# Kernel tuning notes

Hardware: AMD Instinct MI355X
Metric: run time of the kernel (lower is better)

## Reference

```python
import jax, jax.numpy as jnp
import numpy as np

B, T, D, H, O = 64, 2048, 1024, 1024, 1024


def setup_inputs() -> dict:
    key = jax.random.key(0)
    ks = jax.random.split(key, 7)
    std = 1.0 / np.sqrt(H)
    u = lambda k, shape: jax.random.uniform(k, shape, jnp.float32, -std, std)
    return {
        "x": jax.random.normal(ks[0], (B, T, D), jnp.float32),
        "Wx": u(ks[1], (3 * H, D)),
        "bx": u(ks[2], (3 * H,)),
        "Wh": u(ks[3], (3 * H, H)),
        "bh": u(ks[4], (3 * H,)),
        "Wf": u(ks[5], (O, H)),
        "bf": u(ks[6], (O,)),
    }


def _gru_forward(x, Wx, bx, Wh, bh, Wf, bf):
    # Precompute input projections for all timesteps: [B, T, 3H]
    x_proj = jnp.einsum('btd,gd->btg', x, Wx) + bx

    def step(h, xp_t):
        # xp_t: [B, 3H], h: [B, H]
        h_proj = h @ Wh.T + bh
        x_r, x_u, x_n = jnp.split(xp_t, 3, axis=1)
        h_r, h_u, h_n = jnp.split(h_proj, 3, axis=1)
        reset = jax.nn.sigmoid(x_r + h_r)
        update = jax.nn.sigmoid(x_u + h_u)
        new = jnp.tanh(x_n + reset * h_n)
        hy = update * h + (1.0 - update) * new
        return hy, None

    h0 = jnp.zeros((x.shape[0], Wh.shape[1]), x.dtype)
    h_last, _ = jax.lax.scan(step, h0, jnp.swapaxes(x_proj, 0, 1))
    logits = h_last @ Wf.T + bf
    return jax.nn.log_softmax(logits, axis=-1)


def reference(x, Wx, bx, Wh, bh, Wf, bf):
    return _gru_forward(x, Wx, bx, Wh, bh, Wf, bf)
```

## Files before the change

### kernel.cpp

```cpp
#include <hip/hip_runtime.h>
#include <hip/hip_bf16.h>


#define Bb 64
#define Tt 2048
#define Dd 1024
#define Hh 1024

typedef __attribute__((ext_vector_type(8))) short bf16x8;
typedef __attribute__((ext_vector_type(4))) float f32x4;

__device__ __forceinline__ short f2bf(float x) {
    __hip_bfloat16 h = __float2bfloat16(x);
    return __builtin_bit_cast(short, h);
}
__device__ __forceinline__ float bf2f(unsigned short u) {
    return __builtin_bit_cast(float, (unsigned)u << 16);
}
__device__ __forceinline__ bf16x8 pack8(float4 a, float4 b) {
    bf16x8 f;
    f[0] = f2bf(a.x); f[1] = f2bf(a.y); f[2] = f2bf(a.z); f[3] = f2bf(a.w);
    f[4] = f2bf(b.x); f[5] = f2bf(b.y); f[6] = f2bf(b.z); f[7] = f2bf(b.w);
    return f;
}
__device__ __forceinline__ unsigned long long ald64(const void* p) {
    return __hip_atomic_load((const unsigned long long*)p, __ATOMIC_RELAXED,
                             __HIP_MEMORY_SCOPE_AGENT);
}
__device__ __forceinline__ unsigned aldu32(const unsigned* p) {
    return __hip_atomic_load(p, __ATOMIC_RELAXED, __HIP_MEMORY_SCOPE_AGENT);
}

__global__ void wcvt(const float* __restrict__ a, unsigned short* __restrict__ o, long n) {
    long i = ((long)blockIdx.x * blockDim.x + threadIdx.x) * 8;
    long stride = (long)gridDim.x * blockDim.x * 8;
    for (; i < n; i += stride)
        *(bf16x8*)(o + i) = pack8(*(const float4*)(a + i), *(const float4*)(a + i + 4));
}

__global__ __launch_bounds__(256)
void xp_gemm(const float* __restrict__ x, const unsigned short* __restrict__ Wxb,
             unsigned short* __restrict__ xp, int t0) {
    __shared__ unsigned short As[64][40];
    const int tid = threadIdx.x;
    const int wave = tid >> 6, l = tid & 63, lm = l & 15, lk = l >> 4;
    const int slot = blockIdx.y;
    const int t = t0 + slot;
    const int n0w = blockIdx.x * 128 + wave * 32;

    f32x4 acc[4][2] = {};
#pragma unroll 1
    for (int k0 = 0; k0 < 1024; k0 += 32) {
        __syncthreads();
        {
            const int r = tid >> 2, kq = (tid & 3) * 8;
            const float* p = x + (size_t)r * Tt * Dd + (size_t)t * Dd + k0 + kq;
            *(bf16x8*)&As[r][kq] = pack8(*(const float4*)p, *(const float4*)(p + 4));
        }
        __syncthreads();
        bf16x8 bfr[2];
#pragma unroll
        for (int nt = 0; nt < 2; ++nt)
            bfr[nt] = *(const bf16x8*)(Wxb + (size_t)(n0w + nt * 16 + lm) * 1024 + k0 + lk * 8);
#pragma unroll
        for (int mt = 0; mt < 4; ++mt) {
            const bf16x8 af = *(const bf16x8*)&As[mt * 16 + lm][lk * 8];
            acc[mt][0] = __builtin_amdgcn_mfma_f32_16x16x32_bf16(af, bfr[0], acc[mt][0], 0, 0, 0);
            acc[mt][1] = __builtin_amdgcn_mfma_f32_16x16x32_bf16(af, bfr[1], acc[mt][1], 0, 0, 0);
        }
    }
#pragma unroll
    for (int mt = 0; mt < 4; ++mt)
#pragma unroll
        for (int nt = 0; nt < 2; ++nt)
#pragma unroll
            for (int i = 0; i < 4; ++i) {
                const int b = mt * 16 + lk * 4 + i;
                const int n = n0w + nt * 16 + lm;
                xp[((size_t)slot * 64 + b) * 3072 + n] = (unsigned short)f2bf(acc[mt][nt][i]);
            }
}

__global__ __launch_bounds__(512, 2)
void gru_scan6(const float* __restrict__ Wh, const float* __restrict__ bx,
               const float* __restrict__ bh, unsigned short* __restrict__ hl2,
               unsigned short* __restrict__ hmall,
               float* __restrict__ hstate, float* __restrict__ hfinal,
               const unsigned short* __restrict__ xp, int t0, int tend) {
    const int tid = threadIdx.x;
    const int w = tid >> 6, l = tid & 63, lm = l & 15, lk = l >> 4;
    const int bid = blockIdx.x;
    const int g = bid & 7, c = bid >> 3;
    const int bg0 = g * 8, j0 = c * 32;
    const int kb = w * 128;

    __shared__ float comb[8][32][100];
    __shared__ float bxv[96], bhv[96];

    if (tid < 96) {
        const int g3 = tid >> 5, jj = tid & 31;
        bxv[tid] = bx[g3 * 1024 + j0 + jj];
        bhv[tid] = bh[g3 * 1024 + j0 + jj];
    }
    const int grow = tid >> 4, jp = (tid & 15) * 2;
    float hp0 = 0.f, hp1 = 0.f;
    if (tid < 128) {
        const float2 h2 = *(const float2*)(hstate + (size_t)(bg0 + grow) * 1024 + j0 + jp);
        hp0 = h2.x; hp1 = h2.y;
    }

    bf16x8 wf[6][4];
#pragma unroll
    for (int nt = 0; nt < 6; ++nt) {
        const int n96 = nt * 16 + lm, g3 = n96 >> 5, jj = n96 & 31;
        const float* rp = Wh + (size_t)(g3 * 1024 + j0 + jj) * 1024 + kb + lk * 8;
#pragma unroll
        for (int ks = 0; ks < 4; ++ks)
            wf[nt][ks] = pack8(*(const float4*)(rp + ks * 32), *(const float4*)(rp + ks * 32 + 4));
    }
    __syncthreads();

    unsigned xa0 = 0, xa1 = 0, xa2 = 0, xb0 = 0, xb1 = 0, xb2 = 0;
    if (tid < 128) {
        const unsigned short* xr = xp + ((size_t)0 * 64 + bg0 + grow) * 3072 + j0 + jp;
        xa0 = *(const unsigned*)(xr);
        xa1 = *(const unsigned*)(xr + 1024);
        xa2 = *(const unsigned*)(xr + 2048);
    }

    const int row_a = (lm < 8) ? lm : 7;
    unsigned long long rr0, rr1, rr2, rr3, rr4, rr5, rr6, rr7;
    int useMall = 0;

#define L2LOAD(P)                                                              \
    asm volatile(                                                              \
        "global_load_dwordx2 %[a0], %[ad], off sc0\n\t"                        \
        "global_load_dwordx2 %[a1], %[ad], off offset:8 sc0\n\t"               \
        "global_load_dwordx2 %[a2], %[ad], off offset:64 sc0\n\t"              \
        "global_load_dwordx2 %[a3], %[ad], off offset:72 sc0\n\t"              \
        "global_load_dwordx2 %[a4], %[ad], off offset:128 sc0\n\t"             \
        "global_load_dwordx2 %[a5], %[ad], off offset:136 sc0\n\t"             \
        "global_load_dwordx2 %[a6], %[ad], off offset:192 sc0\n\t"             \
        "global_load_dwordx2 %[a7], %[ad], off offset:200 sc0\n\t"             \
        "s_waitcnt vmcnt(0)"                                                   \
        : [a0] "=&v"(rr0), [a1] "=&v"(rr1), [a2] "=&v"(rr2), [a3] "=&v"(rr3),  \
          [a4] "=&v"(rr4), [a5] "=&v"(rr5), [a6] "=&v"(rr6), [a7] "=&v"(rr7)   \
        : [ad] "v"(P)                                                          \
        : "memory")

#pragma unroll 1
    for (int t = t0; t < tend; ++t) {
        const size_t hoff = (size_t)(t & 1) * 65536 + (size_t)g * 8192
                            + (size_t)row_a * 1024 + kb + lk * 8;
        const unsigned long long TAGM = 0x0000000100000001ull;
        const unsigned long long tagrep =
            (unsigned long long)((unsigned)(t >> 1) & 1u) * TAGM;

        if (!useMall) {
            const unsigned short* pl = hl2 + hoff;
            int spins = 0;
            for (;;) {
                L2LOAD(pl);
                const unsigned long long bad =
                    ((rr0 ^ tagrep) | (rr1 ^ tagrep) | (rr2 ^ tagrep) | (rr3 ^ tagrep) |
                     (rr4 ^ tagrep) | (rr5 ^ tagrep) | (rr6 ^ tagrep) | (rr7 ^ tagrep)) & TAGM;
                if (__builtin_expect(__all(bad == 0), 1)) break;
                if (++spins > 256) { useMall = 1; break; }
            }
        }
        if (useMall) {
            const unsigned short* pm = hmall + hoff;
            for (;;) {
                rr0 = ald64(pm);       rr1 = ald64(pm + 4);
                rr2 = ald64(pm + 32);  rr3 = ald64(pm + 36);
                rr4 = ald64(pm + 64);  rr5 = ald64(pm + 68);
                rr6 = ald64(pm + 96);  rr7 = ald64(pm + 100);
                const unsigned long long bad =
                    ((rr0 ^ tagrep) | (rr1 ^ tagrep) | (rr2 ^ tagrep) | (rr3 ^ tagrep) |
                     (rr4 ^ tagrep) | (rr5 ^ tagrep) | (rr6 ^ tagrep) | (rr7 ^ tagrep)) & TAGM;
                if (__builtin_expect(__all(bad == 0), 1)) break;
            }
        }

        if (tid < 128 && t + 1 < tend) {
            const unsigned short* xr = xp + ((size_t)(t + 1 - t0) * 64 + bg0 + grow) * 3072 + j0 + jp;
            xb0 = *(const unsigned*)(xr);
            xb1 = *(const unsigned*)(xr + 1024);
            xb2 = *(const unsigned*)(xr + 2048);
        }

        f32x4 acc[6] = {};
#define KSTEP(KA, KB, KS)                                                       \
        do {                                                                    \
            struct U { unsigned long long a, b; } u{KA, KB};                    \
            const bf16x8 af = __builtin_bit_cast(bf16x8, u);                    \
            _Pragma("unroll")                                                   \
            for (int nt = 0; nt < 6; ++nt)                                      \
                acc[nt] = __builtin_amdgcn_mfma_f32_16x16x32_bf16(              \
                    af, wf[nt][KS], acc[nt], 0, 0, 0);                          \
        } while (0)
        KSTEP(rr0, rr1, 0); KSTEP(rr2, rr3, 1); KSTEP(rr4, rr5, 2); KSTEP(rr6, rr7, 3);
#undef KSTEP

        if (lk < 2) {
#pragma unroll
            for (int nt = 0; nt < 6; ++nt)
#pragma unroll
                for (int i = 0; i < 4; ++i)
                    comb[w][lk * 4 + i][nt * 16 + lm] = acc[nt][i];
        }
        asm volatile("s_waitcnt lgkmcnt(0)\ns_barrier" ::: "memory");

        if (tid < 128) {
            float s00 = 0, s10 = 0, s20 = 0, s01 = 0, s11 = 0, s21 = 0;
#pragma unroll
            for (int ww = 0; ww < 8; ++ww) {
                s00 += comb[ww][grow][jp];      s01 += comb[ww][grow][jp + 1];
                s10 += comb[ww][grow][32 + jp]; s11 += comb[ww][grow][32 + jp + 1];
                s20 += comb[ww][grow][64 + jp]; s21 += comb[ww][grow][64 + jp + 1];
            }
            const float xr0 = bf2f((unsigned short)xa0) + bxv[jp];
            const float xr1 = bf2f((unsigned short)(xa0 >> 16)) + bxv[jp + 1];
            const float xu0 = bf2f((unsigned short)xa1) + bxv[32 + jp];
            const float xu1 = bf2f((unsigned short)(xa1 >> 16)) + bxv[32 + jp + 1];
            const float xn0 = bf2f((unsigned short)xa2) + bxv[64 + jp];
            const float xn1 = bf2f((unsigned short)(xa2 >> 16)) + bxv[64 + jp + 1];
            const float r0 = 1.0f / (1.0f + __expf(-(xr0 + s00 + bhv[jp])));
            const float r1 = 1.0f / (1.0f + __expf(-(xr1 + s01 + bhv[jp + 1])));
            const float u0 = 1.0f / (1.0f + __expf(-(xu0 + s10 + bhv[32 + jp])));
            const float u1 = 1.0f / (1.0f + __expf(-(xu1 + s11 + bhv[32 + jp + 1])));
            const float z0 = xn0 + r0 * (s20 + bhv[64 + jp]);
            const float z1 = xn1 + r1 * (s21 + bhv[64 + jp + 1]);
            const float e0 = __expf(2.0f * z0), e1 = __expf(2.0f * z1);
            const float n0 = 1.0f - 2.0f / (e0 + 1.0f);
            const float n1 = 1.0f - 2.0f / (e1 + 1.0f);
            const float hy0 = u0 * hp0 + (1.0f - u0) * n0;
            const float hy1 = u1 * hp1 + (1.0f - u1) * n1;
            hp0 = hy0; hp1 = hy1;
            const unsigned tagn = ((unsigned)(t + 1) >> 1) & 1u;
            const unsigned v0 = ((unsigned)(unsigned short)f2bf(hy0) & 0xFFFEu) | tagn;
            const unsigned pk = ((unsigned)(unsigned short)f2bf(hy1) << 16) | v0;
            const size_t soff = (size_t)((t + 1) & 1) * 65536 + (size_t)g * 8192
                                + (size_t)grow * 1024 + j0 + jp;
            *(volatile unsigned*)(hl2 + soff) = pk;
            __hip_atomic_store((unsigned*)(hmall + soff), pk, __ATOMIC_RELAXED,
                               __HIP_MEMORY_SCOPE_AGENT);
            if (t == tend - 1)
                *(float2*)(hstate + (size_t)(bg0 + grow) * 1024 + j0 + jp) = make_float2(hy0, hy1);
            if (t == Tt - 1)
                *(float2*)(hfinal + (size_t)(bg0 + grow) * 1024 + j0 + jp) = make_float2(hy0, hy1);
            xa0 = xb0; xa1 = xb1; xa2 = xb2;
        }
        asm volatile("s_barrier" ::: "memory");
    }
#undef L2LOAD
}

template <bool RING>
__global__ __launch_bounds__(256, 1)
void gru_scan(const float* __restrict__ x,
              const float* __restrict__ Wx, const float* __restrict__ bx,
              const float* __restrict__ Wh, const float* __restrict__ bh,
              unsigned short* __restrict__ hbuf, float* __restrict__ hfinal,
              unsigned short* __restrict__ ring, unsigned* __restrict__ flags) {
    const int tid = threadIdx.x;
    const int w   = tid >> 6;
    const int l   = tid & 63;
    const int bid = blockIdx.x;
    const int g   = bid & 1;
    const int c   = bid >> 1;
    const int bg0 = g * 32;
    const int j0  = c * 8;

    __shared__ float comb[4][32][24];
    __shared__ float hp[32][8];
    __shared__ float bxv[24], bhv[24];

    hp[tid >> 3][tid & 7] = 0.0f;
    if (tid < 24) {
        const int gate = tid >> 3, jj = tid & 7;
        bxv[tid] = bx[gate * 1024 + j0 + jj];
        bhv[tid] = bh[gate * 1024 + j0 + jj];
    }

    const int lm = l & 15;
    const int lk = l >> 4;
    const int wb = w * 512;
    bf16x8 bfr[2][16];
    {
        const float* Wbase = (w < 2) ? Wx : Wh;
        const int krel = (w < 2) ? wb : (wb - 1024);
#pragma unroll
        for (int nt = 0; nt < 2; ++nt) {
            int row24 = nt * 16 + lm;
            if (row24 > 23) row24 = 23;
            const int gate = row24 >> 3, jj = row24 & 7;
            const float* rp = Wbase + (size_t)(gate * 1024 + j0 + jj) * 1024 + krel + lk * 8;
#pragma unroll
            for (int ks = 0; ks < 16; ++ks) {
                float4 a = *(const float4*)(rp + ks * 32);
                float4 b = *(const float4*)(rp + ks * 32 + 4);
                bfr[nt][ks] = pack8(a, b);
            }
        }
    }
    __syncthreads();

    if (RING) {
        if (tid < 128) {
            const int e = c * 256 + tid * 2;
            const int rl = e >> 10, col = e & 1023;
#pragma unroll
            for (int s = 0; s < 4; ++s) {
                const float2 xv = *(const float2*)(x + ((size_t)(bg0 + rl) * Tt + s) * Dd + col);
                unsigned pk = (unsigned)(unsigned short)f2bf(xv.x)
                            | ((unsigned)(unsigned short)f2bf(xv.y) << 16);
                __hip_atomic_store((unsigned*)(ring + (size_t)s * 65536
                                               + (size_t)(bg0 + rl) * 1024 + col),
                                   pk, __ATOMIC_RELAXED, __HIP_MEMORY_SCOPE_AGENT);
            }
        }
        asm volatile("s_waitcnt vmcnt(0)" ::: "memory");
        __syncthreads();
        if (tid == 0)
            __hip_atomic_store(&flags[g * 128 + c], 1u, __ATOMIC_RELAXED,
                               __HIP_MEMORY_SCOPE_AGENT);
        if (tid < 128) {
            const unsigned* f = flags + g * 128 + tid;
            while (aldu32(f) < 1u) __builtin_amdgcn_s_sleep(1);
        }
        asm volatile("" ::: "memory");
        __syncthreads();
    }

#pragma unroll 1
    for (int t = 0; t < Tt; ++t) {
        const unsigned short* hcur = hbuf + (size_t)(t & 1) * Bb * Hh;

        if (RING && tid < 128) {
            const int sp = t + 4;
            if (sp < Tt) {
                const int e = c * 256 + tid * 2;
                const int rl = e >> 10, col = e & 1023;
                const float2 xv = *(const float2*)(x + ((size_t)(bg0 + rl) * Tt + sp) * Dd + col);
                unsigned pk = (unsigned)(unsigned short)f2bf(xv.x)
                            | ((unsigned)(unsigned short)f2bf(xv.y) << 16);
                __hip_atomic_store((unsigned*)(ring + (size_t)(sp & 7) * 65536
                                               + (size_t)(bg0 + rl) * 1024 + col),
                                   pk, __ATOMIC_RELAXED, __HIP_MEMORY_SCOPE_AGENT);
            }
        }

        if (w >= 2 && t > 0) {
            const unsigned tgt = (unsigned)(t + 1);
            const unsigned* f0 = flags + g * 128 + l;
            const unsigned* f1 = f0 + 64;
            while (aldu32(f0) < tgt || aldu32(f1) < tgt) __builtin_amdgcn_s_sleep(1);
        }
        asm volatile("" ::: "memory");

        f32x4 acc[2][2] = {};
        if (RING || w >= 2) {
            const unsigned short* src;
            int colb;
            if (w < 2) { src = ring + (size_t)(t & 7) * 65536; colb = wb; }
            else       { src = hcur;                           colb = wb - 1024; }
#pragma unroll
            for (int half = 0; half < 2; ++half) {
                unsigned long long stg[8][2][2];
#pragma unroll
                for (int k8 = 0; k8 < 8; ++k8) {
                    const int ks = half * 8 + k8;
#pragma unroll
                    for (int mt = 0; mt < 2; ++mt) {
                        const unsigned short* p = src + (size_t)(bg0 + mt * 16 + lm) * 1024
                                                  + colb + ks * 32 + lk * 8;
                        stg[k8][mt][0] = ald64(p);
                        stg[k8][mt][1] = ald64(p + 4);
                    }
                }
#pragma unroll
                for (int k8 = 0; k8 < 8; ++k8) {
                    const int ks = half * 8 + k8;
#pragma unroll
                    for (int mt = 0; mt < 2; ++mt) {
                        struct { unsigned long long a, b; } u{stg[k8][mt][0], stg[k8][mt][1]};
                        bf16x8 af = __builtin_bit_cast(bf16x8, u);
                        acc[mt][0] = __builtin_amdgcn_mfma_f32_16x16x32_bf16(af, bfr[0][ks], acc[mt][0], 0, 0, 0);
                        acc[mt][1] = __builtin_amdgcn_mfma_f32_16x16x32_bf16(af, bfr[1][ks], acc[mt][1], 0, 0, 0);
                    }
                }
            }
        } else {
#pragma unroll
            for (int ks = 0; ks < 16; ++ks) {
#pragma unroll
                for (int mt = 0; mt < 2; ++mt) {
                    const size_t row = (size_t)(bg0 + mt * 16 + lm);
                    const size_t off = (row * Tt + t) * Dd + wb + ks * 32 + lk * 8;
                    float4 a = *(const float4*)(x + off);
                    float4 b = *(const float4*)(x + off + 4);
                    bf16x8 af = pack8(a, b);
                    acc[mt][0] = __builtin_amdgcn_mfma_f32_16x16x32_bf16(af, bfr[0][ks], acc[mt][0], 0, 0, 0);
                    acc[mt][1] = __builtin_amdgcn_mfma_f32_16x16x32_bf16(af, bfr[1][ks], acc[mt][1], 0, 0, 0);
                }
            }
        }

#pragma unroll
        for (int mt = 0; mt < 2; ++mt)
#pragma unroll
            for (int nt = 0; nt < 2; ++nt) {
                const int n = nt * 16 + lm;
                if (n < 24) {
#pragma unroll
                    for (int i = 0; i < 4; ++i)
                        comb[w][mt * 16 + lk * 4 + i][n] = acc[mt][nt][i];
                }
            }
        __syncthreads();

        {
            const int b = tid >> 3, j = tid & 7;
            const float rz = comb[0][b][j] + comb[1][b][j] + comb[2][b][j] + comb[3][b][j]
                             + bxv[j] + bhv[j];
            const float uz = comb[0][b][8 + j] + comb[1][b][8 + j] + comb[2][b][8 + j]
                             + comb[3][b][8 + j] + bxv[8 + j] + bhv[8 + j];
            const float nx = comb[0][b][16 + j] + comb[1][b][16 + j] + bxv[16 + j];
            const float nh = comb[2][b][16 + j] + comb[3][b][16 + j] + bhv[16 + j];
            const float r  = 1.0f / (1.0f + __expf(-rz));
            const float u  = 1.0f / (1.0f + __expf(-uz));
            const float zz = nx + r * nh;
            const float e2 = __expf(2.0f * zz);
            const float nv = 1.0f - 2.0f / (e2 + 1.0f);
            const float hold = hp[b][j];
            const float hy = u * hold + (1.0f - u) * nv;
            hp[b][j] = hy;
            unsigned short* hn = hbuf + (size_t)((t + 1) & 1) * Bb * Hh
                                 + (size_t)(bg0 + b) * 1024 + j0 + j;
            __hip_atomic_store(hn, (unsigned short)f2bf(hy), __ATOMIC_RELAXED,
                               __HIP_MEMORY_SCOPE_AGENT);
            if (t == Tt - 1) hfinal[(size_t)(bg0 + b) * 1024 + j0 + j] = hy;
        }
        asm volatile("s_waitcnt vmcnt(0)" ::: "memory");
        __syncthreads();
        if (tid == 0 && t + 1 < Tt)
            __hip_atomic_store(&flags[g * 128 + c], (unsigned)(t + 2), __ATOMIC_RELAXED,
                               __HIP_MEMORY_SCOPE_AGENT);
    }
}

__global__ __launch_bounds__(1024)
void final_kernel(const float* __restrict__ hfinal, const float* __restrict__ Wf,
                  const float* __restrict__ bfv, float* __restrict__ out) {
    const int b = blockIdx.x;
    const int o = threadIdx.x;
    __shared__ float hs[1024];
    __shared__ float redm[16], redsum[16], bcast[2];
    hs[o] = hfinal[(size_t)b * 1024 + o];
    __syncthreads();

    const float* wr = Wf + (size_t)o * 1024;
    float acc = bfv[o];
#pragma unroll 4
    for (int k = 0; k < 1024; k += 4) {
        float4 wv = *(const float4*)(wr + k);
        acc += hs[k] * wv.x + hs[k + 1] * wv.y + hs[k + 2] * wv.z + hs[k + 3] * wv.w;
    }

    float m = acc;
#pragma unroll
    for (int off = 32; off > 0; off >>= 1) m = fmaxf(m, __shfl_xor(m, off));
    if ((o & 63) == 0) redm[o >> 6] = m;
    __syncthreads();
    if (o == 0) {
        float mm = redm[0];
#pragma unroll
        for (int i = 1; i < 16; ++i) mm = fmaxf(mm, redm[i]);
        bcast[0] = mm;
    }
    __syncthreads();
    const float bm = bcast[0];
    float s = __expf(acc - bm);
#pragma unroll
    for (int off = 32; off > 0; off >>= 1) s += __shfl_xor(s, off);
    if ((o & 63) == 0) redsum[o >> 6] = s;
    __syncthreads();
    if (o == 0) {
        float ss = 0.0f;
        for (int i = 0; i < 16; ++i) ss += redsum[i];
        bcast[1] = logf(ss);
    }
    __syncthreads();
    out[(size_t)b * 1024 + o] = acc - bm - bcast[1];
}

extern "C" void kernel_launch(void* const* d_in, const int* in_sizes, int n_in,
                              void* d_out, int out_size, void* d_ws, size_t ws_size,
                              hipStream_t stream) {
    (void)in_sizes; (void)n_in; (void)out_size;
    const float* x   = (const float*)d_in[0];
    const float* Wx  = (const float*)d_in[1];
    const float* bx  = (const float*)d_in[2];
    const float* Wh  = (const float*)d_in[3];
    const float* bh  = (const float*)d_in[4];
    const float* Wf  = (const float*)d_in[5];
    const float* bfv = (const float*)d_in[6];
    float* out = (float*)d_out;
    char* ws = (char*)d_ws;

    const size_t HL = 1024;
    const size_t HM = HL + 262144;
    const size_t HS = HM + 262144;
    const size_t HF = HS + 262144;
    const size_t WX = HF + 262144;
    const size_t XP = WX + 6291456;
    size_t avail = (ws_size > XP) ? (ws_size - XP) : 0;
    long Wl = (long)(avail / 393216);
    if (Wl > 2048) Wl = 2048;
    const int W = (int)Wl;

    if (W >= 32) {
        unsigned short* hl2   = (unsigned short*)(ws + HL);
        unsigned short* hmall = (unsigned short*)(ws + HM);
        float* hstate         = (float*)(ws + HS);
        float* hfinal         = (float*)(ws + HF);
        unsigned short* Wxb   = (unsigned short*)(ws + WX);
        unsigned short* xp    = (unsigned short*)(ws + XP);

        hipMemsetAsync(ws + HL, 0x00, 131072, stream);
        hipMemsetAsync(ws + HL + 131072, 0xFF, 131072, stream);
        hipMemsetAsync(ws + HM, 0x00, 131072, stream);
        hipMemsetAsync(ws + HM + 131072, 0xFF, 131072, stream);
        hipMemsetAsync(ws + HS, 0x00, 262144, stream);
        wcvt<<<1536, 256, 0, stream>>>(Wx, (unsigned short*)Wxb, 3L * 1024 * 1024);
        for (int t0 = 0; t0 < Tt; t0 += W) {
            const int Wc = (Tt - t0 < W) ? (Tt - t0) : W;
            xp_gemm<<<dim3(24, Wc), 256, 0, stream>>>(x, Wxb, xp, t0);
            gru_scan6<<<256, 512, 0, stream>>>(Wh, bx, bh, hl2, hmall, hstate,
                                               hfinal, xp, t0, t0 + Wc);
        }
        final_kernel<<<64, 1024, 0, stream>>>(hfinal, Wf, bfv, out);
    } else {
        unsigned* flags      = (unsigned*)ws;
        unsigned short* hbuf = (unsigned short*)(ws + 1024);
        float* hfinal        = (float*)(ws + 1024 + 262144);
        unsigned short* ring = (unsigned short*)(ws + 1024 + 262144 + 262144);
        const size_t need_ring = 1024 + 262144 + 262144 + (size_t)8 * 131072;
        const bool use_ring = (ws_size >= need_ring);

        hipMemsetAsync(d_ws, 0, 1024 + (size_t)Bb * Hh * 2, stream);
        if (use_ring)
            gru_scan<true><<<256, 256, 0, stream>>>(x, Wx, bx, Wh, bh, hbuf, hfinal, ring, flags);
        else
            gru_scan<false><<<256, 256, 0, stream>>>(x, Wx, bx, Wh, bh, hbuf, hfinal, ring, flags);
        final_kernel<<<64, 1024, 0, stream>>>(hfinal, Wf, bfv, out);
    }
}
```

Measured before the change: 10.18 ms.

## Map scan blocks to batch groups by XCC and widen tagged h loads

At startup each scan block reads its hardware XCC id and claims a slot through atomic counters. When every XCC gets exactly 32 blocks, blocks on the same XCC share one batch group, so the h exchange and tag polling stay within one L2. Otherwise it falls back to the old blockIdx mapping. The tagged h loads become dwordx4, the spin limit before falling back to MALL is raised, and an s_sleep is added to the MALL polling loop. The cost is a grid-wide startup barrier per chunk, which assumes all 256 blocks are co-resident, plus a small registration array whose size has to cover the number of chunks.

```diff
diff --git a/kernel.cpp b/kernel.cpp
--- a/kernel.cpp
+++ b/kernel.cpp
@@ -9,6 +9,7 @@
 
 typedef __attribute__((ext_vector_type(8))) short bf16x8;
 typedef __attribute__((ext_vector_type(4))) float f32x4;
+typedef __attribute__((ext_vector_type(4))) unsigned int u32x4;
 
 __device__ __forceinline__ short f2bf(float x) {
     __hip_bfloat16 h = __float2bfloat16(x);
@@ -82,20 +83,40 @@
 }
 
 __global__ __launch_bounds__(512, 2)
-void gru_scan6(const float* __restrict__ Wh, const float* __restrict__ bx,
+void gru_scan8(const float* __restrict__ Wh, const float* __restrict__ bx,
                const float* __restrict__ bh, unsigned short* __restrict__ hl2,
                unsigned short* __restrict__ hmall,
                float* __restrict__ hstate, float* __restrict__ hfinal,
-               const unsigned short* __restrict__ xp, int t0, int tend) {
+               const unsigned short* __restrict__ xp, unsigned* __restrict__ reg,
+               int t0, int tend) {
     const int tid = threadIdx.x;
     const int w = tid >> 6, l = tid & 63, lm = l & 15, lk = l >> 4;
-    const int bid = blockIdx.x;
-    const int g = bid & 7, c = bid >> 3;
+
+    __shared__ float comb[8][32][100];
+    __shared__ float bxv[96], bhv[96];
+    __shared__ unsigned s_gc;
+
+    if (tid == 0) {
+        unsigned xcc;
+        asm volatile("s_getreg_b32 %0, hwreg(HW_REG_XCC_ID)" : "=s"(xcc));
+        xcc &= 7u;
+        unsigned r = __hip_atomic_fetch_add(&reg[xcc], 1u, __ATOMIC_RELAXED,
+                                            __HIP_MEMORY_SCOPE_AGENT);
+        __hip_atomic_fetch_add(&reg[8], 1u, __ATOMIC_RELEASE, __HIP_MEMORY_SCOPE_AGENT);
+        while (__hip_atomic_load(&reg[8], __ATOMIC_ACQUIRE, __HIP_MEMORY_SCOPE_AGENT) < 256u)
+            __builtin_amdgcn_s_sleep(8);
+        bool bal = (r < 32u);
+        for (int i = 0; i < 8; ++i)
+            bal = bal && (__hip_atomic_load(&reg[i], __ATOMIC_RELAXED,
+                                            __HIP_MEMORY_SCOPE_AGENT) == 32u);
+        const unsigned g = bal ? xcc : (blockIdx.x & 7u);
+        const unsigned c = bal ? r : (blockIdx.x >> 3);
+        s_gc = (g << 8) | c;
+    }
+    __syncthreads();
+    const int g = (s_gc >> 8) & 7, c = s_gc & 255;
     const int bg0 = g * 8, j0 = c * 32;
     const int kb = w * 128;
-
-    __shared__ float comb[8][32][100];
-    __shared__ float bxv[96], bhv[96];
 
     if (tid < 96) {
         const int g3 = tid >> 5, jj = tid & 31;
@@ -129,56 +150,56 @@
     }
 
     const int row_a = (lm < 8) ? lm : 7;
-    unsigned long long rr0, rr1, rr2, rr3, rr4, rr5, rr6, rr7;
+    u32x4 f0, f1, f2, f3;
     int useMall = 0;
 
-#define L2LOAD(P)                                                              \
+#define L2LOAD4(P)                                                             \
     asm volatile(                                                              \
-        "global_load_dwordx2 %[a0], %[ad], off sc0\n\t"                        \
-        "global_load_dwordx2 %[a1], %[ad], off offset:8 sc0\n\t"               \
-        "global_load_dwordx2 %[a2], %[ad], off offset:64 sc0\n\t"              \
-        "global_load_dwordx2 %[a3], %[ad], off offset:72 sc0\n\t"              \
-        "global_load_dwordx2 %[a4], %[ad], off offset:128 sc0\n\t"             \
-        "global_load_dwordx2 %[a5], %[ad], off offset:136 sc0\n\t"             \
-        "global_load_dwordx2 %[a6], %[ad], off offset:192 sc0\n\t"             \
-        "global_load_dwordx2 %[a7], %[ad], off offset:200 sc0\n\t"             \
+        "global_load_dwordx4 %[r0], %[ad], off sc0\n\t"                        \
+        "global_load_dwordx4 %[r1], %[ad], off offset:64 sc0\n\t"              \
+        "global_load_dwordx4 %[r2], %[ad], off offset:128 sc0\n\t"             \
+        "global_load_dwordx4 %[r3], %[ad], off offset:192 sc0\n\t"             \
         "s_waitcnt vmcnt(0)"                                                   \
-        : [a0] "=&v"(rr0), [a1] "=&v"(rr1), [a2] "=&v"(rr2), [a3] "=&v"(rr3),  \
-          [a4] "=&v"(rr4), [a5] "=&v"(rr5), [a6] "=&v"(rr6), [a7] "=&v"(rr7)   \
+        : [r0] "=&v"(f0), [r1] "=&v"(f1), [r2] "=&v"(f2), [r3] "=&v"(f3)       \
         : [ad] "v"(P)                                                          \
         : "memory")
+#define MLOAD4(P)                                                              \
+    do {                                                                       \
+        struct UU { unsigned long long a, b; };                                \
+        UU u0{ald64(P), ald64((P) + 4)};                                       \
+        UU u1{ald64((P) + 32), ald64((P) + 36)};                               \
+        UU u2{ald64((P) + 64), ald64((P) + 68)};                               \
+        UU u3{ald64((P) + 96), ald64((P) + 100)};                              \
+        f0 = __builtin_bit_cast(u32x4, u0);                                    \
+        f1 = __builtin_bit_cast(u32x4, u1);                                    \
+        f2 = __builtin_bit_cast(u32x4, u2);                                    \
+        f3 = __builtin_bit_cast(u32x4, u3);                                    \
+    } while (0)
+#define TAG4(F) (((F)[0] ^ tg) | ((F)[1] ^ tg) | ((F)[2] ^ tg) | ((F)[3] ^ tg))
 
 #pragma unroll 1
     for (int t = t0; t < tend; ++t) {
         const size_t hoff = (size_t)(t & 1) * 65536 + (size_t)g * 8192
                             + (size_t)row_a * 1024 + kb + lk * 8;
-        const unsigned long long TAGM = 0x0000000100000001ull;
-        const unsigned long long tagrep =
-            (unsigned long long)((unsigned)(t >> 1) & 1u) * TAGM;
+        const unsigned tg = (unsigned)(t >> 1) & 1u;
 
         if (!useMall) {
             const unsigned short* pl = hl2 + hoff;
             int spins = 0;
             for (;;) {
-                L2LOAD(pl);
-                const unsigned long long bad =
-                    ((rr0 ^ tagrep) | (rr1 ^ tagrep) | (rr2 ^ tagrep) | (rr3 ^ tagrep) |
-                     (rr4 ^ tagrep) | (rr5 ^ tagrep) | (rr6 ^ tagrep) | (rr7 ^ tagrep)) & TAGM;
-                if (__builtin_expect(__all(bad == 0), 1)) break;
-                if (++spins > 256) { useMall = 1; break; }
+                L2LOAD4(pl);
+                const unsigned bad = (TAG4(f0) | TAG4(f1) | TAG4(f2) | TAG4(f3)) & 1u;
+                if (__builtin_expect(__all((int)(bad == 0u)), 1)) break;
+                if (++spins > 512) { useMall = 1; break; }
             }
         }
         if (useMall) {
             const unsigned short* pm = hmall + hoff;
             for (;;) {
-                rr0 = ald64(pm);       rr1 = ald64(pm + 4);
-                rr2 = ald64(pm + 32);  rr3 = ald64(pm + 36);
-                rr4 = ald64(pm + 64);  rr5 = ald64(pm + 68);
-                rr6 = ald64(pm + 96);  rr7 = ald64(pm + 100);
-                const unsigned long long bad =
-                    ((rr0 ^ tagrep) | (rr1 ^ tagrep) | (rr2 ^ tagrep) | (rr3 ^ tagrep) |
-                     (rr4 ^ tagrep) | (rr5 ^ tagrep) | (rr6 ^ tagrep) | (rr7 ^ tagrep)) & TAGM;
-                if (__builtin_expect(__all(bad == 0), 1)) break;
+                MLOAD4(pm);
+                const unsigned bad = (TAG4(f0) | TAG4(f1) | TAG4(f2) | TAG4(f3)) & 1u;
+                if (__builtin_expect(__all((int)(bad == 0u)), 1)) break;
+                __builtin_amdgcn_s_sleep(1);
             }
         }
 
@@ -190,16 +211,15 @@
         }
 
         f32x4 acc[6] = {};
-#define KSTEP(KA, KB, KS)                                                       \
+#define KSTEP(F, KS)                                                            \
         do {                                                                    \
-            struct U { unsigned long long a, b; } u{KA, KB};                    \
-            const bf16x8 af = __builtin_bit_cast(bf16x8, u);                    \
+            const bf16x8 af = __builtin_bit_cast(bf16x8, F);                    \
             _Pragma("unroll")                                                   \
             for (int nt = 0; nt < 6; ++nt)                                      \
                 acc[nt] = __builtin_amdgcn_mfma_f32_16x16x32_bf16(              \
                     af, wf[nt][KS], acc[nt], 0, 0, 0);                          \
         } while (0)
-        KSTEP(rr0, rr1, 0); KSTEP(rr2, rr3, 1); KSTEP(rr4, rr5, 2); KSTEP(rr6, rr7, 3);
+        KSTEP(f0, 0); KSTEP(f1, 1); KSTEP(f2, 2); KSTEP(f3, 3);
 #undef KSTEP
 
         if (lk < 2) {
@@ -216,21 +236,21 @@
 #pragma unroll
             for (int ww = 0; ww < 8; ++ww) {
                 s00 += comb[ww][grow][jp];      s01 += comb[ww][grow][jp + 1];
-                s10 += comb[ww][grow][32 + jp]; s11 += comb[ww][grow][32 + jp + 1];
-                s20 += comb[ww][grow][64 + jp]; s21 += comb[ww][grow][64 + jp + 1];
+                s10 += comb[ww][grow][32 + jp]; s11 += comb[ww][grow][33 + jp];
+                s20 += comb[ww][grow][64 + jp]; s21 += comb[ww][grow][65 + jp];
             }
             const float xr0 = bf2f((unsigned short)xa0) + bxv[jp];
             const float xr1 = bf2f((unsigned short)(xa0 >> 16)) + bxv[jp + 1];
             const float xu0 = bf2f((unsigned short)xa1) + bxv[32 + jp];
-            const float xu1 = bf2f((unsigned short)(xa1 >> 16)) + bxv[32 + jp + 1];
+            const float xu1 = bf2f((unsigned short)(xa1 >> 16)) + bxv[33 + jp];
             const float xn0 = bf2f((unsigned short)xa2) + bxv[64 + jp];
-            const float xn1 = bf2f((unsigned short)(xa2 >> 16)) + bxv[64 + jp + 1];
+            const float xn1 = bf2f((unsigned short)(xa2 >> 16)) + bxv[65 + jp];
             const float r0 = 1.0f / (1.0f + __expf(-(xr0 + s00 + bhv[jp])));
             const float r1 = 1.0f / (1.0f + __expf(-(xr1 + s01 + bhv[jp + 1])));
             const float u0 = 1.0f / (1.0f + __expf(-(xu0 + s10 + bhv[32 + jp])));
-            const float u1 = 1.0f / (1.0f + __expf(-(xu1 + s11 + bhv[32 + jp + 1])));
+            const float u1 = 1.0f / (1.0f + __expf(-(xu1 + s11 + bhv[33 + jp])));
             const float z0 = xn0 + r0 * (s20 + bhv[64 + jp]);
-            const float z1 = xn1 + r1 * (s21 + bhv[64 + jp + 1]);
+            const float z1 = xn1 + r1 * (s21 + bhv[65 + jp]);
             const float e0 = __expf(2.0f * z0), e1 = __expf(2.0f * z1);
             const float n0 = 1.0f - 2.0f / (e0 + 1.0f);
             const float n1 = 1.0f - 2.0f / (e1 + 1.0f);
@@ -253,7 +273,9 @@
         }
         asm volatile("s_barrier" ::: "memory");
     }
-#undef L2LOAD
+#undef L2LOAD4
+#undef MLOAD4
+#undef TAG4
 }
 
 template <bool RING>
@@ -509,7 +531,8 @@
     float* out = (float*)d_out;
     char* ws = (char*)d_ws;
 
-    const size_t HL = 1024;
+    const size_t RG = 0;
+    const size_t HL = 4096;
     const size_t HM = HL + 262144;
     const size_t HS = HM + 262144;
     const size_t HF = HS + 262144;
@@ -521,6 +544,7 @@
     const int W = (int)Wl;
 
     if (W >= 32) {
+        unsigned* reg         = (unsigned*)(ws + RG);
         unsigned short* hl2   = (unsigned short*)(ws + HL);
         unsigned short* hmall = (unsigned short*)(ws + HM);
         float* hstate         = (float*)(ws + HS);
@@ -528,17 +552,20 @@
         unsigned short* Wxb   = (unsigned short*)(ws + WX);
         unsigned short* xp    = (unsigned short*)(ws + XP);
 
+        hipMemsetAsync(ws + RG, 0x00, 4096, stream);
         hipMemsetAsync(ws + HL, 0x00, 131072, stream);
         hipMemsetAsync(ws + HL + 131072, 0xFF, 131072, stream);
         hipMemsetAsync(ws + HM, 0x00, 131072, stream);
         hipMemsetAsync(ws + HM + 131072, 0xFF, 131072, stream);
         hipMemsetAsync(ws + HS, 0x00, 262144, stream);
         wcvt<<<1536, 256, 0, stream>>>(Wx, (unsigned short*)Wxb, 3L * 1024 * 1024);
-        for (int t0 = 0; t0 < Tt; t0 += W) {
+        int chunk = 0;
+        for (int t0 = 0; t0 < Tt; t0 += W, ++chunk) {
             const int Wc = (Tt - t0 < W) ? (Tt - t0) : W;
             xp_gemm<<<dim3(24, Wc), 256, 0, stream>>>(x, Wxb, xp, t0);
-            gru_scan6<<<256, 512, 0, stream>>>(Wh, bx, bh, hl2, hmall, hstate,
-                                               hfinal, xp, t0, t0 + Wc);
+            gru_scan8<<<256, 512, 0, stream>>>(Wh, bx, bh, hl2, hmall, hstate,
+                                               hfinal, xp, reg + chunk * 16,
+                                               t0, t0 + Wc);
         }
         final_kernel<<<64, 1024, 0, stream>>>(hfinal, Wf, bfv, out);
     } else {
```

Measured after the change: 10.38 ms. About the same (+2.0%).
